# Optimization experiments

Hardware: AMD Instinct MI355X
Metric: run time of the kernel (lower is better)

## Reference

```python
import jax, jax.numpy as jnp
import numpy as np

R, CH, N, E, C, OUT, ED = 2, 2, 20000, 100000, 256, 256, 16


def setup_inputs() -> dict:
    key = jax.random.key(0)
    ks = jax.random.split(key, 11)
    inv = 1.0 / np.sqrt(C)
    return {
        "x": jax.random.normal(ks[0], (R * CH * N, C), jnp.float32),
        "edge_attr": jax.random.normal(ks[1], (E, ED), jnp.float32),
        "edge_weight": jax.random.uniform(ks[2], (R, CH, E, 1), jnp.float32),
        "lin_W": jax.random.normal(ks[3], (C, C), jnp.float32) * inv,
        "lin_b": jax.random.normal(ks[4], (C,), jnp.float32) * inv,
        "linl_W": jax.random.normal(ks[5], (C, OUT), jnp.float32) * inv,
        "linl_b": jax.random.normal(ks[6], (OUT,), jnp.float32) * inv,
        "linr_W": jax.random.normal(ks[7], (C, OUT), jnp.float32) * inv,
        "bond_W": jax.random.normal(ks[8], (ED, C), jnp.float32) / np.sqrt(ED),
        "bond_b": jax.random.normal(ks[9], (C,), jnp.float32) / np.sqrt(ED),
        "edge_index": jax.random.randint(ks[10], (2, E), 0, N, jnp.int64),
    }


def reference(x, edge_attr, edge_weight, lin_W, lin_b, linl_W, linl_b, linr_W,
              bond_W, bond_b, edge_index):
    # bond encoder: (E, ED) -> (E, C), broadcasts as (1, 1, E, C)
    edge_emb = edge_attr @ bond_W + bond_b
    x_l = x @ lin_W + lin_b                      # (R*CH*N, C)
    ux = x_l.reshape(R, CH, N, C)
    src = edge_index[0]
    dst = edge_index[1]
    # gather + add + GELU (exact/erf, matching torch F.gelu) + weight
    msg = jax.nn.gelu(ux[:, :, src, :] + edge_emb, approximate=False) * edge_weight  # (R,CH,E,C)
    # scatter_mean over edge targets
    sums = jnp.zeros((R, CH, N, C), x.dtype).at[:, :, dst, :].add(msg)
    cnt = jnp.zeros((N,), x.dtype).at[dst].add(1.0)
    out = sums / jnp.maximum(cnt, 1.0)[None, None, :, None]
    out = out.reshape(-1, C)                     # (R*CH*N, C)
    return out @ linl_W + linl_b + x @ linr_W
```

## Files before the change

### kernel.cpp

```cpp
#include <hip/hip_runtime.h>
#include <math.h>

#define NN 20000
#define EE 100000
#define CC 256
#define EDM 16
#define RC 4
#define MTOT (RC * NN)

typedef __attribute__((ext_vector_type(8))) short short8;
typedef __attribute__((ext_vector_type(4))) float floatx4;

__device__ __forceinline__ unsigned short f2bf(float f) {
    union { float f; unsigned u; } v; v.f = f;
    unsigned r = v.u + 0x7FFF + ((v.u >> 16) & 1);
    return (unsigned short)(r >> 16);
}
__device__ __forceinline__ float bf2f(unsigned short h) {
    union { unsigned u; float f; } v; v.u = ((unsigned)h) << 16;
    return v.f;
}

__device__ __forceinline__ float gelu_fast(float v) {
    const float ax = fabsf(v) * 0.70710678118654752f;
    const float t  = __builtin_amdgcn_rcpf(fmaf(0.3275911f, ax, 1.0f));
    const float p  = t * fmaf(t, fmaf(t, fmaf(t, fmaf(t, 1.061405429f,
                                -1.453152027f), 1.421413741f), -0.284496736f),
                              0.254829592f);
    const float e  = __builtin_amdgcn_exp2f(ax * ax * -1.4426950408889634f);
    const float erf_ax = fmaf(-p, e, 1.0f);
    return fmaf(0.5f * fabsf(v), erf_ax, 0.5f * v);
}

#define GLDS16(gp, lp)                                                        \
    __builtin_amdgcn_global_load_lds(                                         \
        (const __attribute__((address_space(1))) unsigned int*)(gp),          \
        (__attribute__((address_space(3))) unsigned int*)(lp), 16, 0, 0)

__global__ void k_prep_count(const float* __restrict__ lin_W,
                             const float* __restrict__ linl_W,
                             const float* __restrict__ linr_W,
                             unsigned short* __restrict__ linWT,
                             unsigned short* __restrict__ WbT,
                             const int* __restrict__ eidx,
                             int* __restrict__ cnt) {
    const int b = blockIdx.x;
    const int t = threadIdx.x;
    if (b < CC) {
        linWT[b * CC + t]      = f2bf(lin_W[t * CC + b]);
        WbT[b * 512 + t]       = f2bf(linl_W[t * CC + b]);
        WbT[b * 512 + 256 + t] = f2bf(linr_W[t * CC + b]);
    } else {
        int e = (b - CC) * 256 + t;
        if (e < EE) atomicAdd(cnt + eidx[EE + e], 1);
    }
}

template <int KTOT, int OUTBF16, int A1BF16>
__global__ __launch_bounds__(256) void k_mmb(const float* __restrict__ A1f,
                                             const unsigned short* __restrict__ A1b,
                                             const float* __restrict__ A2f,
                                             const unsigned short* __restrict__ BT,
                                             const float* __restrict__ bias,
                                             float* __restrict__ Cf,
                                             unsigned short* __restrict__ Cb) {
    __shared__ unsigned short As[128 * 64];
    __shared__ unsigned short Bs[128 * 64];
    const int tid  = threadIdx.x;
    const int lane = tid & 63;
    const int wave = tid >> 6;
    const int wr   = wave >> 1;
    const int wc   = wave & 1;
    const int l15  = lane & 15;
    const int q4   = lane >> 4;
    const int lr8  = lane >> 3;
    const int lc8  = lane & 7;
    const int i0   = blockIdx.x * 128;
    const int n0   = blockIdx.y * 128;

    floatx4 acc[4][4];
#pragma unroll
    for (int mt = 0; mt < 4; mt++)
#pragma unroll
        for (int nt = 0; nt < 4; nt++) acc[mt][nt] = (floatx4)0.0f;

    for (int kc = 0; kc < KTOT; kc += 64) {
        __syncthreads();
        const int first = (kc < 256);
        const int kco   = first ? kc : kc - 256;
#pragma unroll
        for (int it = 0; it < 4; it++) {
            const int op = wave * 4 + it;
            const unsigned short* g =
                BT + (size_t)(n0 + op * 8 + lr8) * KTOT + kc + lc8 * 8;
            GLDS16(g, Bs + op * 512);
        }
        if (A1BF16 && first) {
#pragma unroll
            for (int it = 0; it < 4; it++) {
                const int op = wave * 4 + it;
                const unsigned short* g =
                    A1b + (size_t)(i0 + op * 8 + lr8) * CC + kc + lc8 * 8;
                GLDS16(g, As + op * 512);
            }
        } else {
            const float* af = first ? A1f : A2f;
#pragma unroll
            for (int w = 0; w < 4; w++) {
                const int q  = w * 256 + tid;
                const int r  = q >> 3;
                const int c8 = q & 7;
                const float* s = af + (size_t)(i0 + r) * CC + kco + c8 * 8;
                float4 v0 = *(const float4*)(s);
                float4 v1 = *(const float4*)(s + 4);
                uint4 p;
                p.x = (unsigned)f2bf(v0.x) | ((unsigned)f2bf(v0.y) << 16);
                p.y = (unsigned)f2bf(v0.z) | ((unsigned)f2bf(v0.w) << 16);
                p.z = (unsigned)f2bf(v1.x) | ((unsigned)f2bf(v1.y) << 16);
                p.w = (unsigned)f2bf(v1.z) | ((unsigned)f2bf(v1.w) << 16);
                *(uint4*)(As + r * 64 + c8 * 8) = p;
            }
        }
        __syncthreads();
#pragma unroll
        for (int kk = 0; kk < 64; kk += 32) {
            short8 a[4], b[4];
#pragma unroll
            for (int mt = 0; mt < 4; mt++)
                a[mt] = *(const short8*)(As + (wr * 64 + mt * 16 + l15) * 64 + kk + q4 * 8);
#pragma unroll
            for (int nt = 0; nt < 4; nt++)
                b[nt] = *(const short8*)(Bs + (wc * 64 + nt * 16 + l15) * 64 + kk + q4 * 8);
#pragma unroll
            for (int mt = 0; mt < 4; mt++)
#pragma unroll
                for (int nt = 0; nt < 4; nt++)
                    acc[mt][nt] = __builtin_amdgcn_mfma_f32_16x16x32_bf16(
                        a[mt], b[nt], acc[mt][nt], 0, 0, 0);
        }
    }
#pragma unroll
    for (int nt = 0; nt < 4; nt++) {
        const int col = n0 + wc * 64 + nt * 16 + l15;
        const float bz = bias[col];
#pragma unroll
        for (int mt = 0; mt < 4; mt++) {
#pragma unroll
            for (int r = 0; r < 4; r++) {
                const int row = i0 + wr * 64 + mt * 16 + q4 * 4 + r;
                const float v = acc[mt][nt][r] + bz;
                if (OUTBF16) Cb[(size_t)row * CC + col] = f2bf(v);
                else         Cf[(size_t)row * CC + col] = v;
            }
        }
    }
}

#define SCAN_T 1024
#define SCHUNK 20
__global__ __launch_bounds__(1024) void k_scan(const int* __restrict__ cnt,
                                               int* __restrict__ offs,
                                               int* __restrict__ cursor) {
    __shared__ int ps[SCAN_T];
    const int t = threadIdx.x;
    const int base = t * SCHUNK;
    int s = 0;
#pragma unroll
    for (int i = 0; i < SCHUNK; i++) {
        int idx = base + i;
        if (idx < NN) s += cnt[idx];
    }
    ps[t] = s;
    __syncthreads();
    for (int off = 1; off < SCAN_T; off <<= 1) {
        int v = (t >= off) ? ps[t - off] : 0;
        __syncthreads();
        ps[t] += v;
        __syncthreads();
    }
    int excl = (t == 0) ? 0 : ps[t - 1];
#pragma unroll
    for (int i = 0; i < SCHUNK; i++) {
        int idx = base + i;
        if (idx < NN) {
            offs[idx]   = excl;
            cursor[idx] = excl;
            excl += cnt[idx];
        }
    }
    if (t == SCAN_T - 1) offs[NN] = ps[SCAN_T - 1];
}

__global__ void k_scatter(const int* __restrict__ eidx, int* __restrict__ cursor,
                          int* __restrict__ bucket) {
    int e = blockIdx.x * 256 + threadIdx.x;
    if (e < EE) {
        int d = eidx[EE + e];
        int p = atomicAdd(cursor + d, 1);
        bucket[p] = e;
    }
}

__global__ __launch_bounds__(256) void k_agg(const unsigned short* __restrict__ xlb,
                                             const float* __restrict__ edge_attr,
                                             const float* __restrict__ ew,
                                             const float* __restrict__ bond_W,
                                             const float* __restrict__ bond_b,
                                             const int* __restrict__ eidx,
                                             const int* __restrict__ offs,
                                             const int* __restrict__ bucket,
                                             unsigned short* __restrict__ mean_b) {
    const int n = blockIdx.x;
    const int c = threadIdx.x;
    const int beg = offs[n], end = offs[n + 1];
    const float bb = bond_b[c];
    float bw[EDM];
#pragma unroll
    for (int k = 0; k < EDM; k++) bw[k] = bond_W[k * CC + c];

    float a0 = 0.f, a1 = 0.f, a2 = 0.f, a3 = 0.f;

#pragma unroll 2
    for (int j = beg; j < end; j++) {
        const int e   = bucket[j];
        const int src = eidx[e];
        const float w0 = ew[e];
        const float w1 = ew[EE + e];
        const float w2 = ew[2 * EE + e];
        const float w3 = ew[3 * EE + e];
        const float* ea = edge_attr + (size_t)e * EDM;
        float emb = bb;
#pragma unroll
        for (int k = 0; k < EDM; k++)
            emb = fmaf(ea[k], bw[k], emb);
        const size_t sb = (size_t)src * CC + c;
        float v0 = bf2f(xlb[sb])                       + emb;
        float v1 = bf2f(xlb[sb + (size_t)NN * CC])     + emb;
        float v2 = bf2f(xlb[sb + (size_t)2 * NN * CC]) + emb;
        float v3 = bf2f(xlb[sb + (size_t)3 * NN * CC]) + emb;
        a0 += gelu_fast(v0) * w0;
        a1 += gelu_fast(v1) * w1;
        a2 += gelu_fast(v2) * w2;
        a3 += gelu_fast(v3) * w3;
    }
    const float inv = 1.0f / fmaxf((float)(end - beg), 1.0f);
    const size_t ob = (size_t)n * CC + c;
    mean_b[ob]                       = f2bf(a0 * inv);
    mean_b[ob + (size_t)NN * CC]     = f2bf(a1 * inv);
    mean_b[ob + (size_t)2 * NN * CC] = f2bf(a2 * inv);
    mean_b[ob + (size_t)3 * NN * CC] = f2bf(a3 * inv);
}

extern "C" void kernel_launch(void* const* d_in, const int* in_sizes, int n_in,
                              void* d_out, int out_size, void* d_ws, size_t ws_size,
                              hipStream_t stream) {
    (void)in_sizes; (void)n_in; (void)out_size; (void)ws_size;
    const float* x           = (const float*)d_in[0];
    const float* edge_attr   = (const float*)d_in[1];
    const float* edge_weight = (const float*)d_in[2];
    const float* lin_W       = (const float*)d_in[3];
    const float* lin_b       = (const float*)d_in[4];
    const float* linl_W      = (const float*)d_in[5];
    const float* linl_b      = (const float*)d_in[6];
    const float* linr_W      = (const float*)d_in[7];
    const float* bond_W      = (const float*)d_in[8];
    const float* bond_b      = (const float*)d_in[9];
    const int*   edge_index  = (const int*)d_in[10];

    unsigned short* xlb   = (unsigned short*)d_ws;
    unsigned short* linWT = xlb + (size_t)MTOT * CC;
    unsigned short* WbT   = linWT + CC * CC;
    int* cnt    = (int*)(WbT + CC * 512);
    int* offs   = cnt + NN;
    int* cursor = offs + NN + 1;
    int* bucket = cursor + NN;
    uintptr_t mb_addr = (((uintptr_t)(bucket + EE)) + 255) & ~(uintptr_t)255;
    unsigned short* mean_b = (unsigned short*)mb_addr;

    hipMemsetAsync(cnt, 0, NN * sizeof(int), stream);

    k_prep_count<<<CC + (EE + 255) / 256, 256, 0, stream>>>(
        lin_W, linl_W, linr_W, linWT, WbT, edge_index, cnt);
    k_mmb<256, 1, 0><<<dim3(MTOT / 128, 2), 256, 0, stream>>>(
        x, nullptr, nullptr, linWT, lin_b, nullptr, xlb);
    k_scan<<<1, SCAN_T, 0, stream>>>(cnt, offs, cursor);
    k_scatter<<<(EE + 255) / 256, 256, 0, stream>>>(edge_index, cursor, bucket);
    k_agg<<<NN, 256, 0, stream>>>(xlb, edge_attr, edge_weight, bond_W, bond_b,
                                  edge_index, offs, bucket, mean_b);
    k_mmb<512, 0, 1><<<dim3(MTOT / 128, 2), 256, 0, stream>>>(
        nullptr, mean_b, x, WbT, linl_b, (float*)d_out, nullptr);
}
```

Baseline: 372.5 us.

## Interleave R*CH copies of x_l per node and presort edge src/weights for aggregation

The first GEMM now writes x_l interleaved so the four replica values for a node/channel sit next to each other, letting the aggregation fetch them with one 8-byte load instead of four scattered 2-byte loads. The scatter kernel also stores the source index and the four edge weights in CSR order, so the aggregation reads them contiguously rather than through an indirect lookup. Edge attributes are loaded as float4 vectors, and the erf is replaced with a cheaper rational approximation with fewer operations. The cheaper erf approximation is less accurate, and the scratch arrays reuse the output buffer before the final GEMM overwrites it.

```diff
diff --git a/kernel.cpp b/kernel.cpp
--- a/kernel.cpp
+++ b/kernel.cpp
@@ -16,20 +16,20 @@
     unsigned r = v.u + 0x7FFF + ((v.u >> 16) & 1);
     return (unsigned short)(r >> 16);
 }
-__device__ __forceinline__ float bf2f(unsigned short h) {
-    union { unsigned u; float f; } v; v.u = ((unsigned)h) << 16;
+__device__ __forceinline__ float uif(unsigned u) {
+    union { unsigned u; float f; } v; v.u = u;
     return v.f;
 }
 
-__device__ __forceinline__ float gelu_fast(float v) {
-    const float ax = fabsf(v) * 0.70710678118654752f;
-    const float t  = __builtin_amdgcn_rcpf(fmaf(0.3275911f, ax, 1.0f));
-    const float p  = t * fmaf(t, fmaf(t, fmaf(t, fmaf(t, 1.061405429f,
-                                -1.453152027f), 1.421413741f), -0.284496736f),
-                              0.254829592f);
-    const float e  = __builtin_amdgcn_exp2f(ax * ax * -1.4426950408889634f);
-    const float erf_ax = fmaf(-p, e, 1.0f);
-    return fmaf(0.5f * fabsf(v), erf_ax, 0.5f * v);
+__device__ __forceinline__ float gelu27(float v) {
+    const float z  = fabsf(v) * 0.70710678118654752f;
+    const float P  = fmaf(z, fmaf(z, fmaf(z, fmaf(z, 0.078108f, 0.000972f),
+                           0.230389f), 0.278393f), 1.0f);
+    const float r  = __builtin_amdgcn_rcpf(P);
+    const float r2 = r * r;
+    const float r4 = r2 * r2;
+    const float h  = 0.5f * fabsf(v);
+    return fmaf(0.5f, v, fmaf(-h, r4, h));
 }
 
 #define GLDS16(gp, lp)                                                        \
@@ -149,8 +149,13 @@
             for (int r = 0; r < 4; r++) {
                 const int row = i0 + wr * 64 + mt * 16 + q4 * 4 + r;
                 const float v = acc[mt][nt][r] + bz;
-                if (OUTBF16) Cb[(size_t)row * CC + col] = f2bf(v);
-                else         Cf[(size_t)row * CC + col] = v;
+                if (OUTBF16) {
+                    const unsigned rc = (unsigned)row / (unsigned)NN;
+                    const unsigned nn = (unsigned)row - rc * (unsigned)NN;
+                    Cb[((size_t)nn * CC + col) * 4 + rc] = f2bf(v);
+                } else {
+                    Cf[(size_t)row * CC + col] = v;
+                }
             }
         }
     }
@@ -191,22 +196,28 @@
     if (t == SCAN_T - 1) offs[NN] = ps[SCAN_T - 1];
 }
 
-__global__ void k_scatter(const int* __restrict__ eidx, int* __restrict__ cursor,
-                          int* __restrict__ bucket) {
+__global__ void k_scatter(const int* __restrict__ eidx,
+                          const float* __restrict__ ew,
+                          int* __restrict__ cursor,
+                          int* __restrict__ bucket,
+                          int* __restrict__ srcb,
+                          float4* __restrict__ ewb) {
     int e = blockIdx.x * 256 + threadIdx.x;
     if (e < EE) {
         int d = eidx[EE + e];
         int p = atomicAdd(cursor + d, 1);
         bucket[p] = e;
-    }
-}
-
-__global__ __launch_bounds__(256) void k_agg(const unsigned short* __restrict__ xlb,
+        srcb[p]   = eidx[e];
+        ewb[p]    = make_float4(ew[e], ew[EE + e], ew[2 * EE + e], ew[3 * EE + e]);
+    }
+}
+
+__global__ __launch_bounds__(256) void k_agg(const unsigned short* __restrict__ xlb4,
                                              const float* __restrict__ edge_attr,
-                                             const float* __restrict__ ew,
+                                             const float4* __restrict__ ewb,
                                              const float* __restrict__ bond_W,
                                              const float* __restrict__ bond_b,
-                                             const int* __restrict__ eidx,
+                                             const int* __restrict__ srcb,
                                              const int* __restrict__ offs,
                                              const int* __restrict__ bucket,
                                              unsigned short* __restrict__ mean_b) {
@@ -222,26 +233,29 @@
 
 #pragma unroll 2
     for (int j = beg; j < end; j++) {
-        const int e   = bucket[j];
-        const int src = eidx[e];
-        const float w0 = ew[e];
-        const float w1 = ew[EE + e];
-        const float w2 = ew[2 * EE + e];
-        const float w3 = ew[3 * EE + e];
-        const float* ea = edge_attr + (size_t)e * EDM;
+        const int e     = bucket[j];
+        const int src   = srcb[j];
+        const float4 w  = ewb[j];
+        const float4* ea4 = (const float4*)(edge_attr + (size_t)e * EDM);
+        const float4 q0 = ea4[0], q1 = ea4[1], q2 = ea4[2], q3 = ea4[3];
         float emb = bb;
-#pragma unroll
-        for (int k = 0; k < EDM; k++)
-            emb = fmaf(ea[k], bw[k], emb);
-        const size_t sb = (size_t)src * CC + c;
-        float v0 = bf2f(xlb[sb])                       + emb;
-        float v1 = bf2f(xlb[sb + (size_t)NN * CC])     + emb;
-        float v2 = bf2f(xlb[sb + (size_t)2 * NN * CC]) + emb;
-        float v3 = bf2f(xlb[sb + (size_t)3 * NN * CC]) + emb;
-        a0 += gelu_fast(v0) * w0;
-        a1 += gelu_fast(v1) * w1;
-        a2 += gelu_fast(v2) * w2;
-        a3 += gelu_fast(v3) * w3;
+        emb = fmaf(q0.x, bw[0],  emb); emb = fmaf(q0.y, bw[1],  emb);
+        emb = fmaf(q0.z, bw[2],  emb); emb = fmaf(q0.w, bw[3],  emb);
+        emb = fmaf(q1.x, bw[4],  emb); emb = fmaf(q1.y, bw[5],  emb);
+        emb = fmaf(q1.z, bw[6],  emb); emb = fmaf(q1.w, bw[7],  emb);
+        emb = fmaf(q2.x, bw[8],  emb); emb = fmaf(q2.y, bw[9],  emb);
+        emb = fmaf(q2.z, bw[10], emb); emb = fmaf(q2.w, bw[11], emb);
+        emb = fmaf(q3.x, bw[12], emb); emb = fmaf(q3.y, bw[13], emb);
+        emb = fmaf(q3.z, bw[14], emb); emb = fmaf(q3.w, bw[15], emb);
+        const uint2 u = *(const uint2*)(xlb4 + ((size_t)src * CC + c) * 4);
+        const float v0 = uif(u.x << 16)          + emb;
+        const float v1 = uif(u.x & 0xffff0000u)  + emb;
+        const float v2 = uif(u.y << 16)          + emb;
+        const float v3 = uif(u.y & 0xffff0000u)  + emb;
+        a0 = fmaf(gelu27(v0), w.x, a0);
+        a1 = fmaf(gelu27(v1), w.y, a1);
+        a2 = fmaf(gelu27(v2), w.z, a2);
+        a3 = fmaf(gelu27(v3), w.w, a3);
     }
     const float inv = 1.0f / fmaxf((float)(end - beg), 1.0f);
     const size_t ob = (size_t)n * CC + c;
@@ -277,6 +291,9 @@
     uintptr_t mb_addr = (((uintptr_t)(bucket + EE)) + 255) & ~(uintptr_t)255;
     unsigned short* mean_b = (unsigned short*)mb_addr;
 
+    float4* ewb = (float4*)d_out;
+    int*    srcb = (int*)(ewb + EE);
+
     hipMemsetAsync(cnt, 0, NN * sizeof(int), stream);
 
     k_prep_count<<<CC + (EE + 255) / 256, 256, 0, stream>>>(
@@ -284,9 +301,10 @@
     k_mmb<256, 1, 0><<<dim3(MTOT / 128, 2), 256, 0, stream>>>(
         x, nullptr, nullptr, linWT, lin_b, nullptr, xlb);
     k_scan<<<1, SCAN_T, 0, stream>>>(cnt, offs, cursor);
-    k_scatter<<<(EE + 255) / 256, 256, 0, stream>>>(edge_index, cursor, bucket);
-    k_agg<<<NN, 256, 0, stream>>>(xlb, edge_attr, edge_weight, bond_W, bond_b,
-                                  edge_index, offs, bucket, mean_b);
+    k_scatter<<<(EE + 255) / 256, 256, 0, stream>>>(edge_index, edge_weight,
+                                                    cursor, bucket, srcb, ewb);
+    k_agg<<<NN, 256, 0, stream>>>(xlb, edge_attr, ewb, bond_W, bond_b,
+                                  srcb, offs, bucket, mean_b);
     k_mmb<512, 0, 1><<<dim3(MTOT / 128, 2), 256, 0, stream>>>(
         nullptr, mean_b, x, WbT, linl_b, (float*)d_out, nullptr);
 }
```

Result: no change. 376.1 us (+1.0%).
